# Optimization experiments

Measured on AMD Instinct MI355X. Metric: run time of the kernel, lower is better.

Reference implementation:

```python
import jax, jax.numpy as jnp
import numpy as np

D_MODEL = 1024
NUM_HEADS = 16
D_HEAD = D_MODEL // NUM_HEADS  # 64
LAMBDA_INIT = 0.8
EPS = 1e-5


def setup_inputs() -> dict:
    key = jax.random.key(0)
    ks = jax.random.split(key, 10)
    B, N = 2, 2048
    # Xavier-uniform-ish scale for the projection weights
    def xav(k, shape):
        fan_in, fan_out = shape[0], shape[1]
        lim = np.sqrt(6.0 / (fan_in + fan_out))
        return jax.random.uniform(k, shape, jnp.float32, -lim, lim)
    return {
        "X": jax.random.normal(ks[0], (B, N, D_MODEL), jnp.float32),
        "Wq": xav(ks[1], (D_MODEL, 2 * D_MODEL)),
        "Wk": xav(ks[2], (D_MODEL, 2 * D_MODEL)),
        "Wv": xav(ks[3], (D_MODEL, 2 * D_MODEL)),
        "Wo": xav(ks[4], (2 * D_MODEL, D_MODEL)),
        "lambda_q1": jax.random.normal(ks[5], (NUM_HEADS, D_HEAD), jnp.float32),
        "lambda_k1": jax.random.normal(ks[6], (NUM_HEADS, D_HEAD), jnp.float32),
        "lambda_q2": jax.random.normal(ks[7], (NUM_HEADS, D_HEAD), jnp.float32),
        "lambda_k2": jax.random.normal(ks[8], (NUM_HEADS, D_HEAD), jnp.float32),
        "rms_scale": jnp.ones((2 * D_HEAD,), jnp.float32),
    }


def reference(X, Wq, Wk, Wv, Wo, lambda_q1, lambda_k1, lambda_q2, lambda_k2, rms_scale):
    B, N, _ = X.shape
    H, Dh = NUM_HEADS, D_HEAD
    # projections -> [B, H, N, 2*Dh]
    Q = (X @ Wq).reshape(B, N, H, 2 * Dh).transpose(0, 2, 1, 3)
    K = (X @ Wk).reshape(B, N, H, 2 * Dh).transpose(0, 2, 1, 3)
    V = (X @ Wv).reshape(B, N, H, 2 * Dh).transpose(0, 2, 1, 3)
    Q1, Q2 = Q[..., :Dh], Q[..., Dh:]
    K1, K2 = K[..., :Dh], K[..., Dh:]
    # learned lambda per head
    lam = (jnp.exp(jnp.sum(lambda_q1 * lambda_k1, -1))
           - jnp.exp(jnp.sum(lambda_q2 * lambda_k2, -1))
           + LAMBDA_INIT)  # [H]
    scaling = 1.0 / np.sqrt(Dh)
    causal = jnp.tril(jnp.ones((N, N), bool))  # [N, N]
    neg_inf = jnp.float32(-jnp.inf)
    A1 = jnp.einsum('bhqd,bhkd->bhqk', Q1, K1) * scaling
    A2 = jnp.einsum('bhqd,bhkd->bhqk', Q2, K2) * scaling
    A1 = jnp.where(causal, A1, neg_inf)
    A2 = jnp.where(causal, A2, neg_inf)
    attn = jax.nn.softmax(A1, axis=-1) - lam[None, :, None, None] * jax.nn.softmax(A2, axis=-1)
    O = jnp.einsum('bhqk,bhkd->bhqd', attn, V)  # [B, H, N, 2*Dh]
    # per-(batch,head,pos) RMSNorm over the 2*Dh channel dim
    rms = jnp.sqrt(jnp.mean(O * O, axis=-1, keepdims=True) + EPS)
    O = O / rms * rms_scale
    O = O * (1.0 - LAMBDA_INIT)
    O = O.transpose(0, 2, 1, 3).reshape(B, N, H * 2 * Dh)
    return O @ Wo
```

## Files before the change

### kernel.cpp

```cpp
#include <hip/hip_runtime.h>
#include <hip/hip_bf16.h>

#define DM   1024
#define NH   16
#define DH   64
#define NSEQ 2048
#define NBATCH 2
#define ROWS (NBATCH*NSEQ)
#define QKVN (2*DM)
#define STR3 (3*DM*2)

typedef __attribute__((ext_vector_type(8))) short short8;
typedef __attribute__((ext_vector_type(4))) float f32x4;
typedef __attribute__((ext_vector_type(4))) unsigned short u16x4;

__device__ __forceinline__ unsigned short f2bf(float x) {
  union { float f; unsigned u; } v; v.f = x;
  unsigned r = v.u + 0x7FFFu + ((v.u >> 16) & 1u);
  return (unsigned short)(r >> 16);
}

__device__ __forceinline__ float exp2a(float x) {
  float r; asm("v_exp_f32 %0, %1" : "=v"(r) : "v"(x)); return r;
}
__device__ __forceinline__ unsigned cvtpk(float lo, float hi) {
  unsigned d; asm("v_cvt_pk_bf16_f32 %0, %1, %2" : "=v"(d) : "v"(lo), "v"(hi)); return d;
}

__device__ __forceinline__ f32x4 mfma16(short8 a, short8 b, f32x4 c) {
  return __builtin_amdgcn_mfma_f32_16x16x32_bf16(a, b, c, 0, 0, 0);
}

#define GLL(src, dst) \
  __builtin_amdgcn_global_load_lds((const __attribute__((address_space(1))) void*)(src), \
                                   (__attribute__((address_space(3))) void*)(dst), 16, 0, 0)

__global__ void cast_f32_bf16(const float* __restrict__ in, unsigned short* __restrict__ out, int n4) {
  int i = blockIdx.x * blockDim.x + threadIdx.x;
  if (i >= n4) return;
  f32x4 v = *(const f32x4*)(in + (size_t)i * 4);
  u16x4 o;
  #pragma unroll
  for (int j = 0; j < 4; ++j) o[j] = f2bf(v[j]);
  *(u16x4*)(out + (size_t)i * 4) = o;
}

__global__ void transpose_cast_w(const float* __restrict__ in, unsigned short* __restrict__ out,
                                 int R, int C) {
  __shared__ float tile[32][33];
  const int bx = blockIdx.x, by = blockIdx.y;
  const int tx = threadIdx.x, ty = threadIdx.y;
  #pragma unroll
  for (int i = 0; i < 4; ++i)
    tile[ty + i*8][tx] = in[(size_t)(by*32 + ty + i*8) * C + bx*32 + tx];
  __syncthreads();
  #pragma unroll
  for (int i = 0; i < 4; ++i)
    out[(size_t)(bx*32 + ty + i*8) * R + by*32 + tx] = f2bf(tile[tx][ty + i*8]);
}

__global__ void transpose_v(const unsigned short* __restrict__ Vb, unsigned short* __restrict__ Vt) {
  __shared__ unsigned short tile[32][33];
  const int bx = blockIdx.x, by = blockIdx.y;
  const int tx = threadIdx.x, ty = threadIdx.y;
  #pragma unroll
  for (int i = 0; i < 4; ++i)
    tile[ty + i*8][tx] = Vb[(size_t)(by*32 + ty + i*8) * STR3 + bx*32 + tx];
  __syncthreads();
  #pragma unroll
  for (int i = 0; i < 4; ++i) {
    int colg = bx*32 + ty + i*8;
    int rowg = by*32 + tx;
    int hh = colg >> 7, dd = colg & 127;
    int bb = rowg >> 11, nn = rowg & 2047;
    Vt[(size_t)((bb*NH + hh)*128 + dd) * NSEQ + nn] = tile[tx][ty + i*8];
  }
}

__global__ void lam_kernel(const float* __restrict__ lq1, const float* __restrict__ lk1,
                           const float* __restrict__ lq2, const float* __restrict__ lk2,
                           float* __restrict__ lam) {
  int h = threadIdx.x >> 6, lane = threadIdx.x & 63;
  float p1 = lq1[h*64 + lane] * lk1[h*64 + lane];
  float p2 = lq2[h*64 + lane] * lk2[h*64 + lane];
  #pragma unroll
  for (int mk = 32; mk >= 1; mk >>= 1) {
    p1 += __shfl_xor(p1, mk);
    p2 += __shfl_xor(p2, mk);
  }
  if (lane == 0) lam[h] = expf(p1) - expf(p2) + 0.8f;
}

template <typename OT>
__global__ __launch_bounds__(256) void gemm_bt(const unsigned short* __restrict__ A,
                                               const unsigned short* __restrict__ Bt,
                                               OT* __restrict__ C, int M, int N, int K) {
  __shared__ __align__(16) unsigned short As[128*32];
  __shared__ __align__(16) unsigned short Bs[128*32];
  const int tid = threadIdx.x;
  const int w = tid >> 6, lane = tid & 63;
  const int l15 = lane & 15, lg = lane >> 4;
  const int wr = w >> 1, wc = w & 1;

  const unsigned gx = gridDim.x;
  unsigned bid = blockIdx.y * gx + blockIdx.x;
  const unsigned cpx = (gx * gridDim.y) >> 3;
  bid = (bid & 7u) * cpx + (bid >> 3);
  const int m0 = (int)(bid / gx) * 128, n0 = (int)(bid % gx) * 128;

  f32x4 acc[4][4];
  #pragma unroll
  for (int i = 0; i < 4; ++i)
    #pragma unroll
    for (int j = 0; j < 4; ++j) acc[i][j] = f32x4{0.f, 0.f, 0.f, 0.f};

  for (int kt = 0; kt < K; kt += 32) {
    #pragma unroll
    for (int j = 0; j < 2; ++j) {
      int cbase = (j*4 + w) * 64;
      int c = cbase + lane;
      const unsigned short* ga = A + (size_t)(m0 + (c >> 2)) * K + kt + (c & 3) * 8;
      GLL(ga, As + cbase*8);
      const unsigned short* gb = Bt + (size_t)(n0 + (c >> 2)) * K + kt + (c & 3) * 8;
      GLL(gb, Bs + cbase*8);
    }
    __syncthreads();
    short8 af[4], bfr[4];
    #pragma unroll
    for (int m = 0; m < 4; ++m)
      af[m] = *(const short8*)(As + (wr*64 + m*16 + l15) * 32 + lg*8);
    #pragma unroll
    for (int n = 0; n < 4; ++n)
      bfr[n] = *(const short8*)(Bs + (wc*64 + n*16 + l15) * 32 + lg*8);
    #pragma unroll
    for (int m = 0; m < 4; ++m)
      #pragma unroll
      for (int n = 0; n < 4; ++n)
        acc[m][n] = mfma16(af[m], bfr[n], acc[m][n]);
    __syncthreads();
  }

  #pragma unroll
  for (int m = 0; m < 4; ++m)
    #pragma unroll
    for (int n = 0; n < 4; ++n)
      #pragma unroll
      for (int r = 0; r < 4; ++r) {
        int row = m0 + wr*64 + m*16 + lg*4 + r;
        int col = n0 + wc*64 + n*16 + l15;
        if constexpr (sizeof(OT) == 2)
          C[(size_t)row * N + col] = f2bf(acc[m][n][r]);
        else
          C[(size_t)row * N + col] = acc[m][n][r];
      }
}

__global__ __launch_bounds__(256) void diff_attn(const unsigned short* __restrict__ QKV,
                                                 const unsigned short* __restrict__ Vt,
                                                 const float* __restrict__ lam_arr,
                                                 const float* __restrict__ rms_scale,
                                                 unsigned short* __restrict__ O) {
  __shared__ __align__(16) unsigned short Ks[2][64*128];
  __shared__ __align__(16) unsigned short Vs[2][128*64];
  __shared__ __align__(16) unsigned short Plds[4][2][16*64];

  const unsigned bid = blockIdx.x;
  const int xcd = (int)(bid & 7u), idx = (int)(bid >> 3);
  const int bh = xcd * 4 + (idx >> 4);
  const int jj = idx & 15;

  const int b = bh >> 4, h = bh & 15;
  const int w = threadIdx.x >> 6, lane = threadIdx.x & 63;
  const int l15 = lane & 15, lg = lane >> 4;
  const float lam = lam_arr[h];

  const unsigned short* Qb  = QKV + (size_t)(b * NSEQ) * STR3 + h * 128;
  const unsigned short* Kb  = QKV + (size_t)(b * NSEQ) * STR3 + 2048 + h * 128;
  const unsigned short* Vtb = Vt + (size_t)bh * 128 * NSEQ;

  auto stage = [&](int bufi, int key0) {
    #pragma unroll
    for (int j = 0; j < 4; ++j) {
      const int t = j*4 + w;
      {
        const int row = t*4 + (lane >> 4);
        const int ck  = lane & 15;
        const int cks = (ck & 8) | ((ck ^ row) & 7);
        GLL(Kb + (size_t)(key0 + row) * STR3 + cks*8, &Ks[bufi][t*512]);
      }
      {
        const int row = t*8 + (lane >> 3);
        const int ck  = lane & 7;
        const int cks = (ck ^ row) & 7;
        GLL(Vtb + (size_t)row * NSEQ + key0 + cks*8, &Vs[bufi][t*512]);
      }
    }
  };

  char* pb0 = (char*)&Plds[w][0][0];
  char* pb1 = (char*)&Plds[w][1][0];
  const unsigned swz = (unsigned)((l15 & 7) << 4);
  const float qsc = 0.125f * 1.44269504088896340736f;

  for (int pass = 0; pass < 2; ++pass) {
    const int qt = pass ? jj : 31 - jj;
    const int q0 = qt * 64 + w * 16;

    short8 a1[2], a2[2];
    #pragma unroll
    for (int kc = 0; kc < 2; ++kc) {
      const unsigned short* qp = Qb + (size_t)(q0 + l15) * STR3 + kc*32 + lg*8;
      short8 r1 = *(const short8*)qp;
      short8 r2 = *(const short8*)(qp + 64);
      #pragma unroll
      for (int j = 0; j < 8; j += 2) {
        union { unsigned u; float f; } x0, x1, y0, y1;
        x0.u = ((unsigned)(unsigned short)r1[j]) << 16;
        x1.u = ((unsigned)(unsigned short)r1[j+1]) << 16;
        y0.u = ((unsigned)(unsigned short)r2[j]) << 16;
        y1.u = ((unsigned)(unsigned short)r2[j+1]) << 16;
        unsigned d1 = cvtpk(x0.f * qsc, x1.f * qsc);
        unsigned d2 = cvtpk(y0.f * qsc, y1.f * qsc);
        a1[kc][j]   = (short)(unsigned short)(d1 & 0xffffu);
        a1[kc][j+1] = (short)(unsigned short)(d1 >> 16);
        a2[kc][j]   = (short)(unsigned short)(d2 & 0xffffu);
        a2[kc][j+1] = (short)(unsigned short)(d2 >> 16);
      }
    }

    f32x4 o1[8], o2[8];
    #pragma unroll
    for (int i = 0; i < 8; ++i) { o1[i] = f32x4{0,0,0,0}; o2[i] = f32x4{0,0,0,0}; }
    float m1 = -3e38f, l1 = 0.f, m2 = -3e38f, l2 = 0.f;

    stage(0, 0);
    __syncthreads();
    int buf = 0;

    for (int kb = 0; kb <= qt; ++kb) {
      const int key0 = kb * 64;
      if (kb < qt) stage(buf ^ 1, key0 + 64);

      f32x4 st1[4], st2[4];
      #pragma unroll
      for (int nb = 0; nb < 4; ++nb) { st1[nb] = f32x4{0,0,0,0}; st2[nb] = f32x4{0,0,0,0}; }
      __builtin_amdgcn_s_setprio(1);
      #pragma unroll
      for (int nb = 0; nb < 4; ++nb) {
        const int row = nb*16 + l15;
        #pragma unroll
        for (int kc = 0; kc < 2; ++kc) {
          const unsigned short* kp = &Ks[buf][row*128 + (((kc*4 + lg) ^ row) & 7) * 8];
          short8 bk1 = *(const short8*)kp;
          short8 bk2 = *(const short8*)(kp + 64);
          st1[nb] = mfma16(bk1, a1[kc], st1[nb]);
          st2[nb] = mfma16(bk2, a2[kc], st2[nb]);
        }
      }
      __builtin_amdgcn_s_setprio(0);

      if (kb == qt) {
        #pragma unroll
        for (int nb = 0; nb < 4; ++nb)
          #pragma unroll
          for (int r = 0; r < 4; ++r)
            if (key0 + nb*16 + lg*4 + r > q0 + l15) { st1[nb][r] = -3e38f; st2[nb][r] = -3e38f; }
      }

      float tm1 = -3e38f, tm2 = -3e38f;
      #pragma unroll
      for (int nb = 0; nb < 4; ++nb)
        #pragma unroll
        for (int r = 0; r < 4; ++r) {
          tm1 = fmaxf(tm1, st1[nb][r]); tm2 = fmaxf(tm2, st2[nb][r]);
        }
      tm1 = fmaxf(tm1, __shfl_xor(tm1, 16));
      tm1 = fmaxf(tm1, __shfl_xor(tm1, 32));
      tm2 = fmaxf(tm2, __shfl_xor(tm2, 16));
      tm2 = fmaxf(tm2, __shfl_xor(tm2, 32));

      if (__any(tm1 > m1 + 8.f)) {
        const float nm = fmaxf(m1, tm1);
        const float e = exp2a(m1 - nm);
        m1 = nm; l1 *= e;
        float er[4];
        #pragma unroll
        for (int r = 0; r < 4; ++r) er[r] = __shfl(e, lg*4 + r);
        #pragma unroll
        for (int i = 0; i < 8; ++i)
          #pragma unroll
          for (int r = 0; r < 4; ++r) o1[i][r] *= er[r];
      }
      if (__any(tm2 > m2 + 8.f)) {
        const float nm = fmaxf(m2, tm2);
        const float e = exp2a(m2 - nm);
        m2 = nm; l2 *= e;
        float er[4];
        #pragma unroll
        for (int r = 0; r < 4; ++r) er[r] = __shfl(e, lg*4 + r);
        #pragma unroll
        for (int i = 0; i < 8; ++i)
          #pragma unroll
          for (int r = 0; r < 4; ++r) o2[i][r] *= er[r];
      }

      float ts1 = 0.f, ts2 = 0.f;
      #pragma unroll
      for (int nb = 0; nb < 4; ++nb)
        #pragma unroll
        for (int r = 0; r < 4; ++r) {
          st1[nb][r] = exp2a(st1[nb][r] - m1); ts1 += st1[nb][r];
          st2[nb][r] = exp2a(st2[nb][r] - m2); ts2 += st2[nb][r];
        }
      ts1 += __shfl_xor(ts1, 16); ts1 += __shfl_xor(ts1, 32); l1 += ts1;
      ts2 += __shfl_xor(ts2, 16); ts2 += __shfl_xor(ts2, 32); l2 += ts2;

      #pragma unroll
      for (int nb = 0; nb < 4; ++nb) {
        const unsigned off = (unsigned)(l15*128 + nb*32 + lg*8) ^ swz;
        *(uint2*)(pb0 + off) = make_uint2(cvtpk(st1[nb][0], st1[nb][1]),
                                          cvtpk(st1[nb][2], st1[nb][3]));
        *(uint2*)(pb1 + off) = make_uint2(cvtpk(st2[nb][0], st2[nb][1]),
                                          cvtpk(st2[nb][2], st2[nb][3]));
      }
      asm volatile("s_waitcnt lgkmcnt(0)" ::: "memory");
      __builtin_amdgcn_sched_barrier(0);
      short8 pa1[2], pa2[2];
      #pragma unroll
      for (int kc = 0; kc < 2; ++kc) {
        const unsigned off = (unsigned)(l15*128 + kc*64 + lg*16) ^ swz;
        pa1[kc] = *(const short8*)(pb0 + off);
        pa2[kc] = *(const short8*)(pb1 + off);
      }
      __builtin_amdgcn_sched_barrier(0);

      __builtin_amdgcn_s_setprio(1);
      #pragma unroll
      for (int i = 0; i < 8; ++i) {
        const int row = i*16 + l15;
        #pragma unroll
        for (int kc = 0; kc < 2; ++kc) {
          const short8 bv = *(const short8*)(&Vs[buf][row*64 + (((kc*4 + lg) ^ row) & 7) * 8]);
          o1[i] = mfma16(pa1[kc], bv, o1[i]);
          o2[i] = mfma16(pa2[kc], bv, o2[i]);
        }
      }
      __builtin_amdgcn_s_setprio(0);

      __syncthreads();
      buf ^= 1;
    }

    float i1r[4], i2r[4];
    {
      const float inv1 = 1.f / l1, inv2 = 1.f / l2;
      #pragma unroll
      for (int r = 0; r < 4; ++r) {
        i1r[r] = __shfl(inv1, lg*4 + r);
        i2r[r] = __shfl(inv2, lg*4 + r);
      }
    }
    float ov[8][4];
    float ssq[4] = {0.f, 0.f, 0.f, 0.f};
    #pragma unroll
    for (int i = 0; i < 8; ++i)
      #pragma unroll
      for (int r = 0; r < 4; ++r) {
        float v = o1[i][r] * i1r[r] - lam * (o2[i][r] * i2r[r]);
        ov[i][r] = v;
        ssq[r] += v * v;
      }
    #pragma unroll
    for (int r = 0; r < 4; ++r)
      #pragma unroll
      for (int mk = 1; mk < 16; mk <<= 1) ssq[r] += __shfl_xor(ssq[r], mk);
    float rr[4];
    #pragma unroll
    for (int r = 0; r < 4; ++r) rr[r] = rsqrtf(ssq[r] * (1.f/128.f) + 1e-5f) * 0.2f;
    #pragma unroll
    for (int i = 0; i < 8; ++i) {
      const float sc = rms_scale[i*16 + l15];
      #pragma unroll
      for (int r = 0; r < 4; ++r) {
        const int q = q0 + lg*4 + r;
        O[(size_t)(b*NSEQ + q) * QKVN + h*128 + i*16 + l15] = f2bf(ov[i][r] * rr[r] * sc);
      }
    }
  }
}

extern "C" void kernel_launch(void* const* d_in, const int* in_sizes, int n_in,
                              void* d_out, int out_size, void* d_ws, size_t ws_size,
                              hipStream_t stream) {
  (void)in_sizes; (void)n_in; (void)out_size; (void)ws_size;
  const float* X   = (const float*)d_in[0];
  const float* Wq  = (const float*)d_in[1];
  const float* Wk  = (const float*)d_in[2];
  const float* Wv  = (const float*)d_in[3];
  const float* Wo  = (const float*)d_in[4];
  const float* lq1 = (const float*)d_in[5];
  const float* lk1 = (const float*)d_in[6];
  const float* lq2 = (const float*)d_in[7];
  const float* lk2 = (const float*)d_in[8];
  const float* rs  = (const float*)d_in[9];
  float* out = (float*)d_out;

  char* ws = (char*)d_ws;
  const size_t MB = 1ull << 20;
  unsigned short* Xb  = (unsigned short*)(ws);
  unsigned short* Wt  = (unsigned short*)(ws + 8*MB);
  unsigned short* Wot = (unsigned short*)(ws + 20*MB);
  unsigned short* QKV = (unsigned short*)(ws + 24*MB);
  unsigned short* Ob  = (unsigned short*)(ws + 72*MB);
  float*          lamp = (float*)(ws + 88*MB);
  unsigned short* Vt  = (unsigned short*)(ws);

  cast_f32_bf16<<<(ROWS*DM/4 + 255)/256, 256, 0, stream>>>(X, Xb, ROWS*DM/4);
  transpose_cast_w<<<dim3(QKVN/32, DM/32), dim3(32,8), 0, stream>>>(Wq, Wt,             DM, QKVN);
  transpose_cast_w<<<dim3(QKVN/32, DM/32), dim3(32,8), 0, stream>>>(Wk, Wt + 2048*1024, DM, QKVN);
  transpose_cast_w<<<dim3(QKVN/32, DM/32), dim3(32,8), 0, stream>>>(Wv, Wt + 4096*1024, DM, QKVN);
  transpose_cast_w<<<dim3(DM/32, QKVN/32), dim3(32,8), 0, stream>>>(Wo, Wot, QKVN, DM);
  lam_kernel<<<1, 1024, 0, stream>>>(lq1, lk1, lq2, lk2, lamp);

  gemm_bt<unsigned short><<<dim3(STR3/128, ROWS/128), 256, 0, stream>>>(Xb, Wt, QKV, ROWS, STR3, DM);

  transpose_v<<<dim3(QKVN/32, ROWS/32), dim3(32,8), 0, stream>>>(QKV + 4096, Vt);

  diff_attn<<<dim3(512), 256, 0, stream>>>(QKV, Vt, lamp, rs, Ob);

  gemm_bt<float><<<dim3(DM/128, ROWS/128), 256, 0, stream>>>(Ob, Wot, out, ROWS, DM, QKVN);
}
```

Measured before the change: 242.6 us.

## Add 256x256-tile 4-stage pipelined GEMM for the QKV projection

Adds a new GEMM kernel with 256x256 output tiles, 512 threads, and a 4-slot LDS ring filled by direct global-to-LDS loads with explicit vmcnt waits. It replaces the 128x128 gemm_bt for the QKV projection only. The larger tile raises data reuse per loaded byte, and the deeper pipeline is meant to hide global-load latency. In exchange it uses 128 KB of LDS and many accumulator registers per thread, and the grid drops to 24x16 = 384 blocks, which may hurt occupancy and tail balance.

```diff
diff --git a/kernel.cpp b/kernel.cpp
--- a/kernel.cpp
+++ b/kernel.cpp
@@ -35,6 +35,8 @@
   __builtin_amdgcn_global_load_lds((const __attribute__((address_space(1))) void*)(src), \
                                    (__attribute__((address_space(3))) void*)(dst), 16, 0, 0)
 
+#define WAITV(n) asm volatile("s_waitcnt vmcnt(" #n ")" ::: "memory")
+
 __global__ void cast_f32_bf16(const float* __restrict__ in, unsigned short* __restrict__ out, int n4) {
   int i = blockIdx.x * blockDim.x + threadIdx.x;
   if (i >= n4) return;
@@ -89,6 +91,114 @@
     p2 += __shfl_xor(p2, mk);
   }
   if (lane == 0) lam[h] = expf(p1) - expf(p2) + 0.8f;
+}
+
+template <typename OT>
+__global__ __launch_bounds__(512, 2) void gemm256(const unsigned short* __restrict__ A,
+                                                  const unsigned short* __restrict__ Bt,
+                                                  OT* __restrict__ C, int M, int N, int K) {
+  __shared__ __align__(16) unsigned short As[4][256*32];
+  __shared__ __align__(16) unsigned short Bs[4][256*32];
+  const int tid = threadIdx.x;
+  const int wv = tid >> 6, lane = tid & 63;
+  const int l15 = lane & 15, lg = lane >> 4;
+  const int wm = wv >> 2, wn = wv & 3;
+
+  const unsigned gx = gridDim.x;
+  unsigned bid = blockIdx.y * gx + blockIdx.x;
+  const unsigned cpx = (gx * gridDim.y) >> 3;
+  bid = (bid & 7u) * cpx + (bid >> 3);
+  const int m0 = (int)(bid / gx) * 256, n0 = (int)(bid % gx) * 256;
+
+  const int NT = K >> 5;
+
+  int rowS[2], csS[2];
+  #pragma unroll
+  for (int j = 0; j < 2; ++j) {
+    int d = j*512 + tid;
+    int row = d >> 2, c = d & 3;
+    rowS[j] = row;
+    csS[j] = ((c ^ row ^ (row >> 2)) & 3) * 8;
+  }
+
+  auto stage = [&](int slot, int t) {
+    const int kt = t << 5;
+    #pragma unroll
+    for (int j = 0; j < 2; ++j) {
+      const int cb = j*512 + (wv << 6);
+      GLL(A  + (size_t)(m0 + rowS[j]) * K + kt + csS[j], &As[slot][cb*8]);
+      GLL(Bt + (size_t)(n0 + rowS[j]) * K + kt + csS[j], &Bs[slot][cb*8]);
+    }
+  };
+
+  f32x4 acc[8][4];
+  #pragma unroll
+  for (int i = 0; i < 8; ++i)
+    #pragma unroll
+    for (int j = 0; j < 4; ++j) acc[i][j] = f32x4{0.f, 0.f, 0.f, 0.f};
+
+  stage(0, 0); stage(1, 1); stage(2, 2);
+
+  for (int t = 0; t < NT; ++t) {
+    const int rem = NT - 1 - t;
+    if (rem >= 3)      { stage((t+3)&3, t+3); WAITV(12); }
+    else if (rem == 2) { WAITV(8); }
+    else if (rem == 1) { WAITV(4); }
+    else               { WAITV(0); }
+    __builtin_amdgcn_s_barrier();
+    __builtin_amdgcn_sched_barrier(0);
+
+    const unsigned short* as = &As[t & 3][0];
+    const unsigned short* bs = &Bs[t & 3][0];
+    short8 af[4], bf[4];
+    #pragma unroll
+    for (int m = 0; m < 4; ++m) {
+      const int row = wm*128 + m*16 + l15;
+      af[m] = *(const short8*)(as + row*32 + ((lg ^ row ^ (row >> 2)) & 3) * 8);
+    }
+    #pragma unroll
+    for (int n = 0; n < 4; ++n) {
+      const int row = wn*64 + n*16 + l15;
+      bf[n] = *(const short8*)(bs + row*32 + ((lg ^ row ^ (row >> 2)) & 3) * 8);
+    }
+    __builtin_amdgcn_s_setprio(1);
+    #pragma unroll
+    for (int m = 0; m < 4; ++m)
+      #pragma unroll
+      for (int n = 0; n < 4; ++n)
+        acc[m][n] = mfma16(af[m], bf[n], acc[m][n]);
+    __builtin_amdgcn_s_setprio(0);
+
+    short8 af2[4];
+    #pragma unroll
+    for (int m = 0; m < 4; ++m) {
+      const int row = wm*128 + 64 + m*16 + l15;
+      af2[m] = *(const short8*)(as + row*32 + ((lg ^ row ^ (row >> 2)) & 3) * 8);
+    }
+    __builtin_amdgcn_s_setprio(1);
+    #pragma unroll
+    for (int m = 0; m < 4; ++m)
+      #pragma unroll
+      for (int n = 0; n < 4; ++n)
+        acc[4+m][n] = mfma16(af2[m], bf[n], acc[4+m][n]);
+    __builtin_amdgcn_s_setprio(0);
+
+    __builtin_amdgcn_s_barrier();
+  }
+
+  #pragma unroll
+  for (int m = 0; m < 8; ++m)
+    #pragma unroll
+    for (int n = 0; n < 4; ++n)
+      #pragma unroll
+      for (int r = 0; r < 4; ++r) {
+        const int row = m0 + wm*128 + m*16 + lg*4 + r;
+        const int col = n0 + wn*64 + n*16 + l15;
+        if constexpr (sizeof(OT) == 2)
+          C[(size_t)row * N + col] = f2bf(acc[m][n][r]);
+        else
+          C[(size_t)row * N + col] = acc[m][n][r];
+      }
 }
 
 template <typename OT>
@@ -422,7 +532,7 @@
   transpose_cast_w<<<dim3(DM/32, QKVN/32), dim3(32,8), 0, stream>>>(Wo, Wot, QKVN, DM);
   lam_kernel<<<1, 1024, 0, stream>>>(lq1, lk1, lq2, lk2, lamp);
 
-  gemm_bt<unsigned short><<<dim3(STR3/128, ROWS/128), 256, 0, stream>>>(Xb, Wt, QKV, ROWS, STR3, DM);
+  gemm256<unsigned short><<<dim3(STR3/256, ROWS/256), 512, 0, stream>>>(Xb, Wt, QKV, ROWS, STR3, DM);
 
   transpose_v<<<dim3(QKVN/32, ROWS/32), dim3(32,8), 0, stream>>>(QKV + 4096, Vt);
 
```

New measurement: 257.1 us. 1.06x slower.
